# Performance work log

Hardware: AMD Instinct MI355X
Metric: run time of the kernel (lower is better)

The kernel has to match this reference:

```python
import jax, jax.numpy as jnp
import numpy as np

V, E, H, K, PAD = 30000, 128, 256, 32, 0
B, T = 128, 512


def _lstm_dir(x, W_ih, W_hh, b, reverse):
    # x: [B,T,E]; PyTorch LSTM gate order i,f,g,o. b = b_ih + b_hh (mathematically identical).
    Bb, Hh = x.shape[0], W_hh.shape[1]
    xg = jnp.einsum('bte,ge->btg', x, W_ih) + b          # [B,T,4H] precomputed input gates
    xg = jnp.swapaxes(xg, 0, 1)                          # [T,B,4H]

    def step(carry, xg_t):
        h, c = carry
        g = xg_t + h @ W_hh.T
        i, f, gc, o = jnp.split(g, 4, axis=-1)
        c = jax.nn.sigmoid(f) * c + jax.nn.sigmoid(i) * jnp.tanh(gc)
        h = jax.nn.sigmoid(o) * jnp.tanh(c)
        return (h, c), h

    init = (jnp.zeros((Bb, Hh), x.dtype), jnp.zeros((Bb, Hh), x.dtype))
    _, hs = jax.lax.scan(step, init, xg, reverse=reverse)
    return jnp.swapaxes(hs, 0, 1)                        # [B,T,H]


def _viterbi(em, mask, start, end, trans):
    # torchcrf-style Viterbi decode. em: [B,T,K], mask: [B,T] bool (mask[:,0] all True).
    Bb, Tt, Kk = em.shape
    score0 = start[None, :] + em[:, 0]                   # [B,K]
    em_t = jnp.swapaxes(em, 0, 1)[1:]                    # [T-1,B,K]
    m_t = jnp.swapaxes(mask, 0, 1)[1:]                   # [T-1,B]

    def step(score, inp):
        e, m = inp
        cand = score[:, :, None] + trans[None] + e[:, None, :]   # [B,K,K]
        nxt = cand.max(axis=1)
        idx = cand.argmax(axis=1).astype(jnp.int32)               # backpointers [B,K]
        score = jnp.where(m[:, None], nxt, score)
        return score, idx

    score, hist = jax.lax.scan(step, score0, (em_t, m_t))         # hist: [T-1,B,K]
    score = score + end[None, :]
    best = jnp.argmax(score, axis=1).astype(jnp.int32)            # [B] tag at seq end
    barange = jnp.arange(Bb)

    def back(b, inp):
        idx, m = inp
        nb = jnp.where(m, idx[barange, b], b)
        return nb, nb

    _, tags_prev = jax.lax.scan(back, best, (hist, m_t), reverse=True)  # [T-1,B]
    tags = jnp.concatenate([tags_prev, best[None]], axis=0)             # [T,B]
    return jnp.swapaxes(tags, 0, 1)                                     # [B,T] int32


def setup_inputs() -> dict:
    key = jax.random.key(0)
    ks = jax.random.split(key, 14)
    s = 0.1
    f32 = jnp.float32
    return {
        'input': jax.random.randint(ks[0], (B, T), 0, V),
        'mask': jnp.ones((B, T), dtype=bool),
        'target': jax.random.randint(ks[1], (B, T), 0, K),
        'embed_table': jax.random.normal(ks[2], (V, E), f32) * s,
        'W_ih_f': jax.random.normal(ks[3], (4 * H, E), f32) * s,
        'W_hh_f': jax.random.normal(ks[4], (4 * H, H), f32) * s,
        'b_f': jax.random.normal(ks[5], (4 * H,), f32) * s,
        'W_ih_b': jax.random.normal(ks[6], (4 * H, E), f32) * s,
        'W_hh_b': jax.random.normal(ks[7], (4 * H, H), f32) * s,
        'b_b': jax.random.normal(ks[8], (4 * H,), f32) * s,
        'linear_w': jax.random.normal(ks[9], (K, 2 * H), f32) * s,
        'linear_b': jax.random.normal(ks[10], (K,), f32) * s,
        'start_trans': jax.random.normal(ks[11], (K,), f32) * s,
        'end_trans': jax.random.normal(ks[12], (K,), f32) * s,
        'transitions': jax.random.normal(ks[13], (K, K), f32) * s,
    }


def reference(input, mask, target, embed_table, W_ih_f, W_hh_f, b_f,
              W_ih_b, W_hh_b, b_b, linear_w, linear_b,
              start_trans, end_trans, transitions):
    # target is only used by loss_fn; forward() is decode, so it is unused here.
    table = embed_table.at[PAD].set(0.0)                 # padding_idx row is zero
    x = table[input]                                     # [B,T,E]
    hf = _lstm_dir(x, W_ih_f, W_hh_f, b_f, reverse=False)
    hb = _lstm_dir(x, W_ih_b, W_hh_b, b_b, reverse=True)
    h = jnp.concatenate([hf, hb], axis=-1)               # [B,T,2H]
    em = jnp.einsum('bth,kh->btk', h, linear_w) + linear_b  # emissions [B,T,K]
    return _viterbi(em, mask, start_trans, end_trans, transitions)
```

## Files before the change

### kernel.cpp

```cpp
#include <hip/hip_runtime.h>
#include <stdint.h>

#define BB 128
#define TT 512
#define EE 128
#define HH 256
#define KK 32
#define ASTRD 386
#define WSTR  388
#define MAGIC 0x13572468

#define OFF_CNT (512ull << 10)
#define OFF_FLG (516ull << 10)
#define OFF_EM  (2ull << 20)

__global__ __launch_bounds__(512, 1) void k_persist(
        const int* __restrict__ tok, const float* __restrict__ table,
        const float* __restrict__ Wihf, const float* __restrict__ Whhf,
        const float* __restrict__ bf,
        const float* __restrict__ Wihb, const float* __restrict__ Whhb,
        const float* __restrict__ bb,
        const float* __restrict__ lw,
        float* __restrict__ hx, int* __restrict__ cnt,
        double* __restrict__ em, int* __restrict__ flags) {
    __shared__ __align__(16) double Ah[16 * ASTRD];
    __shared__ __align__(16) float  Wl[64 * WSTR];
    __shared__ float Gl[16 * 66];
    __shared__ float Lw[2 * 256];

    const int tid  = threadIdx.x;
    const int blk  = blockIdx.x;
    const int grp  = blk & 15;
    const int dir  = grp >> 3;
    const int tile = grp & 7;
    const int hsl  = blk >> 4;
    const int b0   = tile * 16;
    const int u0   = hsl * 16;
    int* mycnt = cnt + grp * 64;

    if (blk == 0 && tid == 0) flags[8] = MAGIC;

    const float* Wih = dir ? Wihb : Wihf;
    const float* Whh = dir ? Whhb : Whhf;
    const float* bia = dir ? bb : bf;

    for (int idx = tid; idx < 64 * 384; idx += 512) {
        int c = idx / 384;
        int k = idx - c * 384;
        int grow = (c >> 4) * HH + u0 + (c & 15);
        float v = (k < EE) ? Wih[(size_t)grow * EE + k]
                           : Whh[(size_t)grow * HH + (k - EE)];
        Wl[c * WSTR + k] = v;
    }
    if (tid < 512) {
        int i = tid;
        Lw[i] = lw[(size_t)(hsl * 2 + (i >> 8)) * (2 * HH) + dir * HH + (i & 255)];
    }

    const int c = tid & 63;
    const int w = tid >> 6;
    const float* WrowL = Wl + c * WSTR;
    const float bias_c = bia[(c >> 4) * HH + u0 + (c & 15)];

    const int er = tid >> 4, eu = tid & 15;
    float c_state = 0.f;
    long guard = 0;
    float xgv[2];

    for (int s = 0; s <= TT; ++s) {
        if (s < TT) {
            const int t = dir ? (TT - 1 - s) : s;
            const int i = tid;
            const int r = i >> 5, e4 = i & 31;
            int tk = tok[(b0 + r) * TT + t];
            float4 v = make_float4(0.f, 0.f, 0.f, 0.f);
            if (tk != 0) v = ((const float4*)(table + (size_t)tk * EE))[e4];
            double2* dst = (double2*)(Ah + r * ASTRD + e4 * 4);
            dst[0] = make_double2((double)v.x, (double)v.y);
            dst[1] = make_double2((double)v.z, (double)v.w);
        }
        __syncthreads();

        if (s < TT) {
            double a0 = 0.0, a1 = 0.0;
            const double* A0 = Ah + (2 * w + 0) * ASTRD;
            const double* A1 = Ah + (2 * w + 1) * ASTRD;
#pragma unroll 4
            for (int k = 0; k < EE; k += 4) {
                float4 wf = *((const float4*)(WrowL + k));
                const double w0 = wf.x, w1 = wf.y, w2 = wf.z, w3 = wf.w;
                double2 q0, q1;
                q0 = *((const double2*)(A0 + k)); q1 = *((const double2*)(A0 + k + 2));
                a0 += q0.x * w0 + q0.y * w1 + q1.x * w2 + q1.y * w3;
                q0 = *((const double2*)(A1 + k)); q1 = *((const double2*)(A1 + k + 2));
                a1 += q0.x * w0 + q0.y * w1 + q1.x * w2 + q1.y * w3;
            }
            xgv[0] = __fadd_rn((float)a0, bias_c);
            xgv[1] = __fadd_rn((float)a1, bias_c);
        }

        if (s > 0 && tid == 0) {
            const int target = 16 * s;
            while (__hip_atomic_load(mycnt, __ATOMIC_RELAXED,
                                     __HIP_MEMORY_SCOPE_AGENT) < target) {
                __builtin_amdgcn_s_sleep(2);
                if (++guard > 100000000L) {
                    __hip_atomic_store(&flags[10], s, __ATOMIC_RELAXED,
                                       __HIP_MEMORY_SCOPE_AGENT);
                    break;
                }
            }
            __threadfence();
        }
        __syncthreads();

        if (s == 0) {
            for (int i = tid; i < 2048; i += 512) {
                int r = i >> 7, u2 = i & 127;
                *((double2*)(Ah + r * ASTRD + EE + u2 * 2)) = make_double2(0.0, 0.0);
            }
        } else {
            const int rp = (s & 1) ^ 1;
            int i = tid;
#pragma unroll
            for (int rep = 0; rep < 4; ++rep, i += 512) {
                int r = i >> 7, u2 = i & 127;
                const unsigned long long* p = (const unsigned long long*)
                    (hx + ((size_t)((rp * 2 + dir) * BB + b0 + r)) * HH + u2 * 2);
                unsigned long long raw = __hip_atomic_load(
                    p, __ATOMIC_RELAXED, __HIP_MEMORY_SCOPE_AGENT);
                union { unsigned long long u; float f[2]; } cv; cv.u = raw;
                *((double2*)(Ah + r * ASTRD + EE + u2 * 2)) =
                    make_double2((double)cv.f[0], (double)cv.f[1]);
            }
        }
        __syncthreads();

        if (s >= 1 && tid < 256) {
            const int d = tid >> 3, sub = tid & 7;
            const int row = d >> 1, kk = d & 1;
            const int t_em = dir ? (TT - s) : (s - 1);
            double p = 0.0;
#pragma unroll
            for (int j = sub * 32; j < sub * 32 + 32; ++j)
                p += Ah[row * ASTRD + EE + j] * (double)Lw[kk * 256 + j];
            p += __shfl_xor(p, 1, 64);
            p += __shfl_xor(p, 2, 64);
            p += __shfl_xor(p, 4, 64);
            if (sub == 0)
                atomicAdd(em + ((size_t)(b0 + row) * TT + t_em) * KK + hsl * 2 + kk, p);
        }
        if (s == TT) break;

        {
            double a0 = 0.0, a1 = 0.0;
            const double* A0 = Ah + (2 * w + 0) * ASTRD + EE;
            const double* A1 = Ah + (2 * w + 1) * ASTRD + EE;
            const float* WhL = WrowL + EE;
#pragma unroll 4
            for (int k = 0; k < HH; k += 4) {
                float4 wf = *((const float4*)(WhL + k));
                const double w0 = wf.x, w1 = wf.y, w2 = wf.z, w3 = wf.w;
                double2 q0, q1;
                q0 = *((const double2*)(A0 + k)); q1 = *((const double2*)(A0 + k + 2));
                a0 += q0.x * w0 + q0.y * w1 + q1.x * w2 + q1.y * w3;
                q0 = *((const double2*)(A1 + k)); q1 = *((const double2*)(A1 + k + 2));
                a1 += q0.x * w0 + q0.y * w1 + q1.x * w2 + q1.y * w3;
            }
            Gl[(2 * w + 0) * 66 + c] = __fadd_rn(xgv[0], (float)a0);
            Gl[(2 * w + 1) * 66 + c] = __fadd_rn(xgv[1], (float)a1);
        }
        __syncthreads();

        if (tid < 256) {
            const float gi = Gl[er * 66 +  0 + eu];
            const float gf = Gl[er * 66 + 16 + eu];
            const float gg = Gl[er * 66 + 32 + eu];
            const float go = Gl[er * 66 + 48 + eu];
            const float si = 1.f / (1.f + expf(-gi));
            const float sf = 1.f / (1.f + expf(-gf));
            const float so = 1.f / (1.f + expf(-go));
            const float tg = tanhf(gg);
            const float cnew = __fadd_rn(__fmul_rn(sf, c_state), __fmul_rn(si, tg));
            c_state = cnew;
            const float hval = __fmul_rn(so, tanhf(cnew));
            __hip_atomic_store(
                hx + ((size_t)(((s & 1) * 2 + dir) * BB + b0 + er)) * HH + u0 + eu,
                hval, __ATOMIC_RELAXED, __HIP_MEMORY_SCOPE_AGENT);
        }

        __syncthreads();
        if (tid == 0) {
            __threadfence();
            __hip_atomic_fetch_add(mycnt, 1, __ATOMIC_RELAXED,
                                   __HIP_MEMORY_SCOPE_AGENT);
        }
    }
}

__global__ __launch_bounds__(64) void k_viterbi(const double* __restrict__ em,
                                                const float* __restrict__ lb,
                                                const float* __restrict__ startt,
                                                const float* __restrict__ endt,
                                                const float* __restrict__ trans,
                                                int* __restrict__ out) {
    const int b = blockIdx.x;
    const int lane = threadIdx.x;
    const int j = lane & 31, half = lane >> 5;
    __shared__ float trs[32][33];
    __shared__ unsigned char hist[TT][32];
    __shared__ int tags[TT];

    for (int idx = lane; idx < 1024; idx += 64)
        trs[idx >> 5][idx & 31] = trans[idx];
    __syncthreads();

    const float lbj = lb[j];
    const double* emb = em + (size_t)b * TT * KK;
    float score = __fadd_rn(startt[j], __fadd_rn((float)emb[j], lbj));

    for (int t = 1; t < TT; ++t) {
        const float e_cur = __fadd_rn((float)emb[(size_t)t * KK + j], lbj);
        float best = -3.4e38f; int bi = 0;
#pragma unroll
        for (int ii = 0; ii < 16; ++ii) {
            int i = half * 16 + ii;
            float sc_i = __shfl(score, i, 64);
            float c1 = __fadd_rn(sc_i, trs[i][j]);
            float cand = __fadd_rn(c1, e_cur);
            if (cand > best) { best = cand; bi = i; }
        }
        float ob = __shfl_xor(best, 32, 64);
        int obi = __shfl_xor(bi, 32, 64);
        if (ob > best || (ob == best && obi < bi)) { best = ob; bi = obi; }
        score = best;
        if (half == 0) hist[t][j] = (unsigned char)bi;
    }

    score = __fadd_rn(score, endt[j]);
    int bj = j; float bs = score;
#pragma unroll
    for (int off = 16; off >= 1; off >>= 1) {
        float os = __shfl_xor(bs, off, 64);
        int oj = __shfl_xor(bj, off, 64);
        if (os > bs || (os == bs && oj < bj)) { bs = os; bj = oj; }
    }
    __syncthreads();
    if (lane == 0) {
        int cur = bj;
        tags[TT - 1] = cur;
        for (int t = TT - 2; t >= 0; --t) { cur = hist[t + 1][cur]; tags[t] = cur; }
    }
    __syncthreads();
    for (int t2 = lane; t2 < TT; t2 += 64) out[b * TT + t2] = tags[t2];
}

__global__ __launch_bounds__(64) void k_final(const int* __restrict__ flags,
                                              int* __restrict__ outp) {
    if (threadIdx.x != 0) return;
    if (flags[8] != MAGIC)   outp[0] = 990000;
    else if (flags[10] != 0) outp[0] = 850000 + flags[10] * 64;
}

extern "C" void kernel_launch(void* const* d_in, const int* in_sizes, int n_in,
                              void* d_out, int out_size, void* d_ws, size_t ws_size,
                              hipStream_t stream) {
    const int*   tok   = (const int*)d_in[0];
    const float* table = (const float*)d_in[3];
    const float* Wihf  = (const float*)d_in[4];
    const float* Whhf  = (const float*)d_in[5];
    const float* bf    = (const float*)d_in[6];
    const float* Wihb  = (const float*)d_in[7];
    const float* Whhb  = (const float*)d_in[8];
    const float* bb    = (const float*)d_in[9];
    const float* lw    = (const float*)d_in[10];
    const float* lb    = (const float*)d_in[11];
    const float* st    = (const float*)d_in[12];
    const float* en    = (const float*)d_in[13];
    const float* tr    = (const float*)d_in[14];

    if (ws_size < (19ull << 20)) return;

    char* ws = (char*)d_ws;
    float*  hx    = (float*)ws;
    int*    cnt   = (int*)(ws + OFF_CNT);
    int*    flags = (int*)(ws + OFF_FLG);
    double* em    = (double*)(ws + OFF_EM);

    hipMemsetAsync(cnt, 0, 8192, stream);
    hipMemsetAsync(em, 0, (size_t)BB * TT * KK * 8, stream);
    k_persist<<<256, 512, 0, stream>>>(tok, table, Wihf, Whhf, bf,
                                       Wihb, Whhb, bb, lw, hx, cnt, em, flags);
    k_viterbi<<<BB, 64, 0, stream>>>(em, lb, st, en, tr, (int*)d_out);
    k_final  <<<1, 64, 0, stream>>>(flags, (int*)d_out);
}
```

Measured before the change: 8.248 ms.

## Use FP64 MFMA for LSTM gate matmuls with runtime layout probe

Replaces the scalar FP64 dot products for the input and recurrent gate projections with 16x16x4 FP64 MFMA instructions on four waves. A startup probe runs test MFMAs to detect the accumulator layout (normal or transposed) and falls back to the old scalar path if neither matches. This targets ALU cost inside the sequential per-step critical path. In exchange, it adds strided LDS loads and leaves half the waves idle during the matmul, and the summation order changes.

```diff
diff --git a/kernel.cpp b/kernel.cpp
--- a/kernel.cpp
+++ b/kernel.cpp
@@ -9,6 +9,8 @@
 #define ASTRD 386
 #define WSTR  388
 #define MAGIC 0x13572468
+
+typedef double f64x4 __attribute__((ext_vector_type(4)));
 
 #define OFF_CNT (512ull << 10)
 #define OFF_FLG (516ull << 10)
@@ -52,20 +54,61 @@
                            : Whh[(size_t)grow * HH + (k - EE)];
         Wl[c * WSTR + k] = v;
     }
-    if (tid < 512) {
+    {
         int i = tid;
         Lw[i] = lw[(size_t)(hsl * 2 + (i >> 8)) * (2 * HH) + dir * HH + (i & 255)];
     }
 
+    const int l = tid & 63;
+    const int w = tid >> 6;
+
+    int mode = 0;
+    {
+        f64x4 z; z[0] = 0.0; z[1] = 0.0; z[2] = 0.0; z[3] = 0.0;
+        double a1 = (double)(l & 15);
+        double b1 = (l == 0) ? 1.0 : 0.0;
+        f64x4 d1 = __builtin_amdgcn_mfma_f64_16x16x4f64(a1, b1, z, 0, 0, 0);
+        double a2 = (double)(l >> 4);
+        double b2 = (l == ((3 << 4) | 5)) ? 1.0 : 0.0;
+        f64x4 d2 = __builtin_amdgcn_mfma_f64_16x16x4f64(a2, b2, z, 0, 0, 0);
+        bool okC = true, okT = true;
+#pragma unroll
+        for (int r = 0; r < 4; ++r) {
+            const int rowC = 4 * (l >> 4) + r;
+            double e1C = ((l & 15) == 0) ? (double)rowC : 0.0;
+            double e2C = ((l & 15) == 5) ? 3.0 : 0.0;
+            okC = okC && (d1[r] == e1C) && (d2[r] == e2C);
+            double e1T = (rowC == 0) ? (double)(l & 15) : 0.0;
+            double e2T = (rowC == 5) ? 3.0 : 0.0;
+            okT = okT && (d1[r] == e1T) && (d2[r] == e2T);
+        }
+        if (__ballot(okC ? 1 : 0) == ~0ull)      mode = 1;
+        else if (__ballot(okT ? 1 : 0) == ~0ull) mode = 2;
+    }
+
     const int c = tid & 63;
-    const int w = tid >> 6;
     const float* WrowL = Wl + c * WSTR;
     const float bias_c = bia[(c >> 4) * HH + u0 + (c & 15)];
+
+    const int kq = l >> 4;
+    const double* Arow = Ah + (l & 15) * ASTRD;
+    const float*  Wb   = Wl + (w * 16 + (l & 15)) * WSTR + kq;
+    int   glIdx[4];
+    float biasv[4];
+#pragma unroll
+    for (int r = 0; r < 4; ++r) {
+        int row_u, col_u;
+        if (mode == 2) { row_u = l & 15; col_u = 4 * kq + r; }
+        else           { row_u = 4 * kq + r; col_u = l & 15; }
+        glIdx[r] = row_u * 66 + w * 16 + col_u;
+        biasv[r] = bia[w * HH + u0 + col_u];
+    }
 
     const int er = tid >> 4, eu = tid & 15;
     float c_state = 0.f;
     long guard = 0;
     float xgv[2];
+    float xgm[4];
 
     for (int s = 0; s <= TT; ++s) {
         if (s < TT) {
@@ -82,21 +125,40 @@
         __syncthreads();
 
         if (s < TT) {
-            double a0 = 0.0, a1 = 0.0;
-            const double* A0 = Ah + (2 * w + 0) * ASTRD;
-            const double* A1 = Ah + (2 * w + 1) * ASTRD;
+            if (mode != 0) {
+                if (w < 4) {
+                    f64x4 ax0; ax0[0]=0.0; ax0[1]=0.0; ax0[2]=0.0; ax0[3]=0.0;
+                    f64x4 ax1 = ax0;
+#pragma unroll 8
+                    for (int kb = 0; kb < 32; kb += 2) {
+                        double a0 = Arow[kb * 4 + kq];
+                        double b0 = (double)Wb[kb * 4];
+                        double a1 = Arow[(kb + 1) * 4 + kq];
+                        double b1 = (double)Wb[(kb + 1) * 4];
+                        ax0 = __builtin_amdgcn_mfma_f64_16x16x4f64(a0, b0, ax0, 0, 0, 0);
+                        ax1 = __builtin_amdgcn_mfma_f64_16x16x4f64(a1, b1, ax1, 0, 0, 0);
+                    }
+#pragma unroll
+                    for (int r = 0; r < 4; ++r)
+                        xgm[r] = __fadd_rn((float)(ax0[r] + ax1[r]), biasv[r]);
+                }
+            } else {
+                double a0 = 0.0, a1 = 0.0;
+                const double* A0 = Ah + (2 * w + 0) * ASTRD;
+                const double* A1 = Ah + (2 * w + 1) * ASTRD;
 #pragma unroll 4
-            for (int k = 0; k < EE; k += 4) {
-                float4 wf = *((const float4*)(WrowL + k));
-                const double w0 = wf.x, w1 = wf.y, w2 = wf.z, w3 = wf.w;
-                double2 q0, q1;
-                q0 = *((const double2*)(A0 + k)); q1 = *((const double2*)(A0 + k + 2));
-                a0 += q0.x * w0 + q0.y * w1 + q1.x * w2 + q1.y * w3;
-                q0 = *((const double2*)(A1 + k)); q1 = *((const double2*)(A1 + k + 2));
-                a1 += q0.x * w0 + q0.y * w1 + q1.x * w2 + q1.y * w3;
-            }
-            xgv[0] = __fadd_rn((float)a0, bias_c);
-            xgv[1] = __fadd_rn((float)a1, bias_c);
+                for (int k = 0; k < EE; k += 4) {
+                    float4 wf = *((const float4*)(WrowL + k));
+                    const double w0 = wf.x, w1 = wf.y, w2 = wf.z, w3 = wf.w;
+                    double2 q0, q1;
+                    q0 = *((const double2*)(A0 + k)); q1 = *((const double2*)(A0 + k + 2));
+                    a0 += q0.x * w0 + q0.y * w1 + q1.x * w2 + q1.y * w3;
+                    q0 = *((const double2*)(A1 + k)); q1 = *((const double2*)(A1 + k + 2));
+                    a1 += q0.x * w0 + q0.y * w1 + q1.x * w2 + q1.y * w3;
+                }
+                xgv[0] = __fadd_rn((float)a0, bias_c);
+                xgv[1] = __fadd_rn((float)a1, bias_c);
+            }
         }
 
         if (s > 0 && tid == 0) {
@@ -152,7 +214,24 @@
         }
         if (s == TT) break;
 
-        {
+        if (mode != 0) {
+            if (w < 4) {
+                f64x4 ah0; ah0[0]=0.0; ah0[1]=0.0; ah0[2]=0.0; ah0[3]=0.0;
+                f64x4 ah1 = ah0;
+#pragma unroll 8
+                for (int kb = 32; kb < 96; kb += 2) {
+                    double a0 = Arow[kb * 4 + kq];
+                    double b0 = (double)Wb[kb * 4];
+                    double a1 = Arow[(kb + 1) * 4 + kq];
+                    double b1 = (double)Wb[(kb + 1) * 4];
+                    ah0 = __builtin_amdgcn_mfma_f64_16x16x4f64(a0, b0, ah0, 0, 0, 0);
+                    ah1 = __builtin_amdgcn_mfma_f64_16x16x4f64(a1, b1, ah1, 0, 0, 0);
+                }
+#pragma unroll
+                for (int r = 0; r < 4; ++r)
+                    Gl[glIdx[r]] = __fadd_rn(xgm[r], (float)(ah0[r] + ah1[r]));
+            }
+        } else {
             double a0 = 0.0, a1 = 0.0;
             const double* A0 = Ah + (2 * w + 0) * ASTRD + EE;
             const double* A1 = Ah + (2 * w + 1) * ASTRD + EE;
```

After: 8.168 ms. Within noise of the previous version (-1.0%).
